# Optimization experiments

Hardware: AMD Instinct MI355X
Metric: run time of the kernel (lower is better)

The kernel has to match this reference:

```python
import jax, jax.numpy as jnp
import numpy as np

NUM_CHIPS = 4
EXPERTS_PER_CHIP = 8
N_EXPERTS = 32            # NUM_CHIPS * EXPERTS_PER_CHIP
TOP_K = 4
SEQ = 1024
HIDDEN = 2048
MAX_TOK = 1024            # max_dispatched_tokens_per_expert
META_LEN = 8


def setup_inputs() -> dict:
    key = jax.random.key(0)
    k1, k2, k3 = jax.random.split(key, 3)
    x = jax.random.normal(k1, (NUM_CHIPS, SEQ, HIDDEN), jnp.float32)
    weights = jax.random.uniform(k2, (NUM_CHIPS, SEQ, TOP_K), jnp.float32)
    indices = jax.random.randint(k3, (NUM_CHIPS, SEQ, TOP_K), 0, N_EXPERTS, jnp.int32)
    return {"x": x, "weights": weights, "indices": indices}


def _dispatch_plan(indices):
    """Compute, for every (chip, token, topk) assignment, its destination slot in the
    global per-expert buffers, replicating the serialized offset-counter loop:
    chips write in order chip0..chipC, and within a chip in (token, topk) order."""
    C, S, K = indices.shape
    N = S * K
    e = indices.reshape(C, N)                                     # expert per assignment
    # per-chip per-expert counts
    counts = jax.vmap(lambda ec: jnp.zeros(N_EXPERTS, jnp.int32).at[ec].add(1))(e)  # [C,E]
    # exclusive prefix sum over chips -> starting offset of each chip within each expert buffer
    chip_off = jnp.cumsum(counts, axis=0) - counts                # [C,E]

    def rank_within_chip(ec, cnt):
        # stable sort groups assignments by expert while preserving (token, topk) order
        order = jnp.argsort(ec, stable=True)
        group_start = (jnp.cumsum(cnt) - cnt)[ec[order]]
        rk_sorted = jnp.arange(N, dtype=jnp.int32) - group_start
        return jnp.zeros(N, jnp.int32).at[order].set(rk_sorted)

    rank = jax.vmap(rank_within_chip)(e, counts)                  # [C,N]
    dst = jnp.take_along_axis(chip_off, e, axis=1) + rank         # slot within expert buffer
    flat = (e * MAX_TOK + dst).reshape(-1)                        # index into (E*MAX_TOK)
    return e, flat, counts


def reference(x, weights, indices):
    C, S, H = x.shape
    K = indices.shape[-1]
    N = S * K
    e, flat, counts = _dispatch_plan(indices)

    # scatter token vectors: each assignment gets a unique slot -> plain set
    x_rep = jnp.repeat(x, K, axis=1).reshape(C * N, H)
    buf = jnp.zeros((N_EXPERTS * MAX_TOK, H), x.dtype).at[flat].set(x_rep)
    buf = buf.reshape(NUM_CHIPS, EXPERTS_PER_CHIP, MAX_TOK, H)

    # metadata: [chip, token, topk, routed_expert, bf16-bits(weight), 0...]
    chip_id = jnp.broadcast_to(jnp.arange(C, dtype=jnp.int32)[:, None], (C, N))
    tok = jnp.broadcast_to(jnp.repeat(jnp.arange(S, dtype=jnp.int32), K)[None, :], (C, N))
    topk = jnp.broadcast_to(jnp.tile(jnp.arange(K, dtype=jnp.int32), S)[None, :], (C, N))
    wbits = jax.lax.bitcast_convert_type(weights.astype(jnp.bfloat16), jnp.int16)
    wbits = wbits.astype(jnp.int32).reshape(C, N)
    md = jnp.stack([chip_id, tok, topk, e, wbits], axis=-1)       # [C,N,5]
    md = jnp.concatenate([md, jnp.zeros((C, N, META_LEN - 5), jnp.int32)], axis=-1)
    meta = jnp.full((N_EXPERTS * MAX_TOK, META_LEN), -1, jnp.int32).at[flat].set(md.reshape(-1, META_LEN))
    meta = meta.reshape(NUM_CHIPS, EXPERTS_PER_CHIP, MAX_TOK, META_LEN)

    experts_counter = counts.sum(axis=0).reshape(NUM_CHIPS, EXPERTS_PER_CHIP)
    return buf, meta, experts_counter
```

## Files before the change

### kernel.cpp

```cpp
#include <hip/hip_runtime.h>
#include <hip/hip_bf16.h>
#include <stdint.h>
#include <string.h>

#define NUM_CHIPS 4
#define N_EXPERTS 32
#define TOP_K 4
#define SEQ 1024
#define HIDDEN 2048
#define MAX_TOK 1024
#define META_LEN 8
#define NPC (SEQ * TOP_K)
#define ROWS (N_EXPERTS * MAX_TOK)
#define BUF_ELEMS ((size_t)ROWS * HIDDEN)
#define META_OFF BUF_ELEMS
#define CNT_OFF (BUF_ELEMS + (size_t)ROWS * META_LEN)

__global__ __launch_bounds__(256) void plan_kernel(const int* __restrict__ idx,
                                                   int* __restrict__ inv,
                                                   float* __restrict__ out) {
    __shared__ int run_base[N_EXPERTS];
    __shared__ int wave_cnt[4][N_EXPERTS];
    __shared__ int wave_base[4][N_EXPERTS];

    const int t = threadIdx.x;
    const int lane = t & 63;
    const int w = t >> 6;

    if (t < N_EXPERTS) run_base[t] = 0;
    __syncthreads();

    for (int c = 0; c < NUM_CHIPS; ++c) {
        for (int chunk = 0; chunk < NPC / 256; ++chunk) {
            const int n = chunk * 256 + t;
            const int e = idx[c * NPC + n];

            if (t < 4 * N_EXPERTS) ((int*)wave_cnt)[t] = 0;
            __syncthreads();

            uint64_t m = ~0ull;
#pragma unroll
            for (int b = 0; b < 5; ++b) {
                uint64_t bb = __ballot((e >> b) & 1);
                m &= ((e >> b) & 1) ? bb : ~bb;
            }
            const uint64_t below = (1ull << lane) - 1ull;
            const int rk = __popcll(m & below);
            if (rk == 0) wave_cnt[w][e] = __popcll(m);
            __syncthreads();

            if (t < N_EXPERTS) {
                int s = run_base[t];
#pragma unroll
                for (int ww = 0; ww < 4; ++ww) {
                    wave_base[ww][t] = s;
                    s += wave_cnt[ww][t];
                }
                run_base[t] = s;
            }
            __syncthreads();

            const int dst = wave_base[w][e] + rk;
            const int flat = e * MAX_TOK + dst;
            inv[flat] = (c << 12) | n;
        }
    }
    __syncthreads();
    if (t < N_EXPERTS) out[CNT_OFF + t] = (float)run_base[t];
}

__global__ __launch_bounds__(256) void scatter_kernel(const float* __restrict__ x,
                                                      const float* __restrict__ wts,
                                                      const int* __restrict__ inv,
                                                      float* __restrict__ out) {
    const int row = blockIdx.x;
    const int t = threadIdx.x;
    const int iv = inv[row];

    float4* dst = (float4*)(out + (size_t)row * HIDDEN);

    if (iv >= 0) {
        const int c = iv >> 12;
        const int n = iv & (NPC - 1);
        const int token = n >> 2;
        const float4* src = (const float4*)(x + ((size_t)c * SEQ + token) * HIDDEN);
#pragma unroll
        for (int i = 0; i < HIDDEN / 4 / 256; ++i)
            dst[t + i * 256] = src[t + i * 256];

        if (t < META_LEN) {
            float v = 0.0f;
            if (t == 0) v = (float)c;
            else if (t == 1) v = (float)token;
            else if (t == 2) v = (float)(n & 3);
            else if (t == 3) v = (float)(row >> 10);
            else if (t == 4) {
                float wv = wts[c * NPC + n];
                uint32_t ub;
                memcpy(&ub, &wv, 4);
                uint32_t lsb = (ub >> 16) & 1u;
                uint32_t bits = (ub + 0x7FFFu + lsb) >> 16;
                v = (float)(int)(short)(uint16_t)bits;
            }
            out[META_OFF + (size_t)row * META_LEN + t] = v;
        }
    } else {
        const float4 z = make_float4(0.f, 0.f, 0.f, 0.f);
#pragma unroll
        for (int i = 0; i < HIDDEN / 4 / 256; ++i)
            dst[t + i * 256] = z;
        if (t < META_LEN)
            out[META_OFF + (size_t)row * META_LEN + t] = -1.0f;
    }
}

extern "C" void kernel_launch(void* const* d_in, const int* in_sizes, int n_in,
                              void* d_out, int out_size, void* d_ws, size_t ws_size,
                              hipStream_t stream) {
    const float* x   = (const float*)d_in[0];
    const float* wts = (const float*)d_in[1];
    const int*   idx = (const int*)d_in[2];
    float* out = (float*)d_out;
    int* inv = (int*)d_ws;

    hipMemsetAsync(inv, 0xFF, (size_t)ROWS * sizeof(int), stream);

    plan_kernel<<<1, 256, 0, stream>>>(idx, inv, out);
    scatter_kernel<<<ROWS, 256, 0, stream>>>(x, wts, inv, out);
}
```

Before: 347.2 us.

## Parallelize dispatch planning across chips and drop the inverse-map memset

The single-block serial planning kernel becomes a per-chip ranking kernel (4 blocks of 1024 threads) and a separate emit kernel that adds the cross-chip offsets and writes the inverse map in parallel. The scatter kernel now tells empty slots apart by comparing each slot against the per-expert totals, so the memset that pre-filled the inverse map is gone. The aim is to shorten the serial 64-iteration planning phase that runs before the bandwidth-bound scatter, at the cost of one extra kernel launch.

```diff
diff --git a/kernel.cpp b/kernel.cpp
--- a/kernel.cpp
+++ b/kernel.cpp
@@ -11,75 +11,106 @@
 #define MAX_TOK 1024
 #define META_LEN 8
 #define NPC (SEQ * TOP_K)
+#define NTOT (NUM_CHIPS * NPC)
 #define ROWS (N_EXPERTS * MAX_TOK)
 #define BUF_ELEMS ((size_t)ROWS * HIDDEN)
 #define META_OFF BUF_ELEMS
 #define CNT_OFF (BUF_ELEMS + (size_t)ROWS * META_LEN)
 
-__global__ __launch_bounds__(256) void plan_kernel(const int* __restrict__ idx,
-                                                   int* __restrict__ inv,
-                                                   float* __restrict__ out) {
+#define WS_RANK 0
+#define WS_CNT  (NTOT)
+#define WS_TOT  (NTOT + 128)
+#define WS_INV  (NTOT + 128 + 32)
+
+__global__ __launch_bounds__(1024) void rank_kernel(const int* __restrict__ idx,
+                                                    int* __restrict__ ws) {
     __shared__ int run_base[N_EXPERTS];
-    __shared__ int wave_cnt[4][N_EXPERTS];
-    __shared__ int wave_base[4][N_EXPERTS];
+    __shared__ int wave_cnt[16][N_EXPERTS];
+    __shared__ int wave_base[16][N_EXPERTS];
 
+    const int c = blockIdx.x;
     const int t = threadIdx.x;
     const int lane = t & 63;
     const int w = t >> 6;
 
+    int e[4];
+#pragma unroll
+    for (int q = 0; q < 4; ++q) e[q] = idx[c * NPC + q * 1024 + t];
+
     if (t < N_EXPERTS) run_base[t] = 0;
     __syncthreads();
 
-    for (int c = 0; c < NUM_CHIPS; ++c) {
-        for (int chunk = 0; chunk < NPC / 256; ++chunk) {
-            const int n = chunk * 256 + t;
-            const int e = idx[c * NPC + n];
+#pragma unroll
+    for (int q = 0; q < 4; ++q) {
+        if (t < 16 * N_EXPERTS) ((int*)wave_cnt)[t] = 0;
+        __syncthreads();
 
-            if (t < 4 * N_EXPERTS) ((int*)wave_cnt)[t] = 0;
-            __syncthreads();
+        uint64_t m = ~0ull;
+#pragma unroll
+        for (int b = 0; b < 5; ++b) {
+            uint64_t bb = __ballot((e[q] >> b) & 1);
+            m &= ((e[q] >> b) & 1) ? bb : ~bb;
+        }
+        const int rk = __popcll(m & ((1ull << lane) - 1ull));
+        if (rk == 0) wave_cnt[w][e[q]] = __popcll(m);
+        __syncthreads();
 
-            uint64_t m = ~0ull;
+        if (t < N_EXPERTS) {
+            int s = run_base[t];
 #pragma unroll
-            for (int b = 0; b < 5; ++b) {
-                uint64_t bb = __ballot((e >> b) & 1);
-                m &= ((e >> b) & 1) ? bb : ~bb;
+            for (int ww = 0; ww < 16; ++ww) {
+                wave_base[ww][t] = s;
+                s += wave_cnt[ww][t];
             }
-            const uint64_t below = (1ull << lane) - 1ull;
-            const int rk = __popcll(m & below);
-            if (rk == 0) wave_cnt[w][e] = __popcll(m);
-            __syncthreads();
+            run_base[t] = s;
+        }
+        __syncthreads();
 
-            if (t < N_EXPERTS) {
-                int s = run_base[t];
-#pragma unroll
-                for (int ww = 0; ww < 4; ++ww) {
-                    wave_base[ww][t] = s;
-                    s += wave_cnt[ww][t];
-                }
-                run_base[t] = s;
-            }
-            __syncthreads();
-
-            const int dst = wave_base[w][e] + rk;
-            const int flat = e * MAX_TOK + dst;
-            inv[flat] = (c << 12) | n;
-        }
+        ws[WS_RANK + c * NPC + q * 1024 + t] = wave_base[w][e[q]] + rk;
     }
     __syncthreads();
-    if (t < N_EXPERTS) out[CNT_OFF + t] = (float)run_base[t];
+    if (t < N_EXPERTS) ws[WS_CNT + c * N_EXPERTS + t] = run_base[t];
+}
+
+__global__ __launch_bounds__(256) void emit_kernel(const int* __restrict__ idx,
+                                                   int* __restrict__ ws,
+                                                   float* __restrict__ out) {
+    __shared__ int cnt_s[NUM_CHIPS * N_EXPERTS];
+    const int t = threadIdx.x;
+    if (t < NUM_CHIPS * N_EXPERTS) cnt_s[t] = ws[WS_CNT + t];
+    __syncthreads();
+
+    const int a = blockIdx.x * 256 + t;
+    const int c = a >> 12;
+    const int n = a & (NPC - 1);
+    const int e = idx[a];
+
+    int off = 0;
+    for (int cc = 0; cc < c; ++cc) off += cnt_s[cc * N_EXPERTS + e];
+    const int dst = off + ws[WS_RANK + a];
+    ws[WS_INV + e * MAX_TOK + dst] = (c << 12) | n;
+
+    if (blockIdx.x == 0 && t < N_EXPERTS) {
+        int s = cnt_s[t] + cnt_s[N_EXPERTS + t] + cnt_s[2 * N_EXPERTS + t] +
+                cnt_s[3 * N_EXPERTS + t];
+        ws[WS_TOT + t] = s;
+        out[CNT_OFF + t] = (float)s;
+    }
 }
 
 __global__ __launch_bounds__(256) void scatter_kernel(const float* __restrict__ x,
                                                       const float* __restrict__ wts,
-                                                      const int* __restrict__ inv,
+                                                      const int* __restrict__ ws,
                                                       float* __restrict__ out) {
     const int row = blockIdx.x;
     const int t = threadIdx.x;
-    const int iv = inv[row];
+    const int e = row >> 10;
+    const int slot = row & (MAX_TOK - 1);
 
     float4* dst = (float4*)(out + (size_t)row * HIDDEN);
 
-    if (iv >= 0) {
+    if (slot < ws[WS_TOT + e]) {
+        const int iv = ws[WS_INV + row];
         const int c = iv >> 12;
         const int n = iv & (NPC - 1);
         const int token = n >> 2;
@@ -93,7 +124,7 @@
             if (t == 0) v = (float)c;
             else if (t == 1) v = (float)token;
             else if (t == 2) v = (float)(n & 3);
-            else if (t == 3) v = (float)(row >> 10);
+            else if (t == 3) v = (float)e;
             else if (t == 4) {
                 float wv = wts[c * NPC + n];
                 uint32_t ub;
@@ -121,10 +152,9 @@
     const float* wts = (const float*)d_in[1];
     const int*   idx = (const int*)d_in[2];
     float* out = (float*)d_out;
-    int* inv = (int*)d_ws;
+    int* ws = (int*)d_ws;
 
-    hipMemsetAsync(inv, 0xFF, (size_t)ROWS * sizeof(int), stream);
-
-    plan_kernel<<<1, 256, 0, stream>>>(idx, inv, out);
-    scatter_kernel<<<ROWS, 256, 0, stream>>>(x, wts, inv, out);
+    rank_kernel<<<NUM_CHIPS, 1024, 0, stream>>>(idx, ws);
+    emit_kernel<<<NTOT / 256, 256, 0, stream>>>(idx, ws, out);
+    scatter_kernel<<<ROWS, 256, 0, stream>>>(x, wts, ws, out);
 }
```

After: 301.0 us. 1.15x faster.
